# Kernel tuning notes

Measured on AMD Instinct MI355X. Metric: run time of the kernel, lower is better.

Reference implementation:

```python
import jax, jax.numpy as jnp
import numpy as np

FREQ_RES = 100.0 / 256.0
NUM_FILTERS = 6
_CFG = [(0.5, 4.0), (4.0, 8.0), (8.0, 12.0), (12.0, 16.0), (16.0, 24.0), (24.0, 30.0)]
BANDS = [(int(a / FREQ_RES), int(b / FREQ_RES)) for a, b in _CFG]  # (start_bin, end_bin)


def _interp_idx(n_src, n_dst):
    # torch F.interpolate bilinear, align_corners=False, along last dim (T dim is identity since same size)
    j = np.arange(n_dst)
    src = np.maximum((j + 0.5) * n_src / n_dst - 0.5, 0.0)
    x0 = np.floor(src).astype(np.int32)
    x1 = np.minimum(x0 + 1, n_src - 1)
    w = (src - x0).astype(np.float32)
    return x0, x1, w


def _gelu(x):
    return jax.nn.gelu(x, approximate=False)


def _forward(spec, centers, widths, gains, align_w, align_b, fc1_w, fc1_b, fc2_w, fc2_b,
             band_gain, gate_w, gate_b, proj_w, proj_b, bn_gamma, bn_beta, bn_mean, bn_var):
    B, C, T, F = spec.shape
    N = NUM_FILTERS
    band_feats = []
    for i, (s, e) in enumerate(BANDS):
        nb = e - s + 1
        sl = spec[:, :, :, s:e + 1]                       # [B,C,T,nb]
        mu = jax.nn.softplus(centers[i]) + s              # [C,N]
        mu = jnp.clip(mu, s, s + nb - 1)
        std = jnp.clip(jax.nn.softplus(widths[i]) + 1e-3, 0.5, 2.0 * nb / N)
        freqs = jnp.arange(nb, dtype=spec.dtype)          # relative bins [nb]
        g = jnp.exp(-0.5 * ((freqs[None, None, :] - mu[:, :, None]) / std[:, :, None]) ** 2)  # [C,N,nb]
        w = gains[i][:, :, None] * g / (g.sum(-1, keepdims=True) + 1e-6)
        filt = jnp.einsum('bctf,cnf->bctn', sl, w)        # [B,C,T,N]
        aligned = jnp.einsum('bctn,dc->bdtn', filt, align_w[i]) + align_b[i][None, :, None, None]
        band_feats.append(aligned)
    band_stack = jnp.stack(band_feats, axis=1)            # [B,6,C,T,N]
    nb_bands = band_stack.shape[1]
    x = band_stack.reshape(B, nb_bands * C, T, N)
    h = _gelu(jnp.einsum('bktn,ok->botn', x, fc1_w) + fc1_b[None, :, None, None])
    attn = jnp.einsum('botn,ko->bktn', h, fc2_w) + fc2_b[None, :, None, None]
    attn = jax.nn.softmax(attn.reshape(B, nb_bands, C, T, N), axis=1)  # softmax over bands
    band_stack = band_stack * attn * band_gain[None, :, None, None, None]
    enhanced = jnp.zeros_like(spec)
    for i, (s, e) in enumerate(BANDS):
        nb = e - s + 1
        narrow = band_stack[:, i]                         # [B,C,T,N]
        x0, x1, wl = _interp_idx(NUM_FILTERS, nb)
        wl = jnp.asarray(wl, dtype=spec.dtype)
        bf = narrow[..., x0] * (1.0 - wl) + narrow[..., x1] * wl   # [B,C,T,nb]
        enhanced = enhanced.at[:, :, :, s:e + 1].add(bf)
    residual = enhanced - spec
    gate = jax.nn.sigmoid(jnp.einsum('bctf,dc->bdtf', residual, gate_w) + gate_b[None, :, None, None])
    enhanced2 = spec + gate * residual
    y = jnp.einsum('bctf,dc->bdtf', enhanced2, proj_w) + proj_b[None, :, None, None]
    y = (y - bn_mean[None, :, None, None]) / jnp.sqrt(bn_var[None, :, None, None] + 1e-5)
    y = y * bn_gamma[None, :, None, None] + bn_beta[None, :, None, None]
    return _gelu(y)


def setup_inputs() -> dict:
    key = jax.random.key(0)
    ks = jax.random.split(key, 8)
    B, C, T, F, N = 64, 3, 3000, 103, NUM_FILTERS
    spec = jax.random.normal(ks[0], (B, C, T, F), dtype=jnp.float32)
    centers = jnp.stack([jnp.broadcast_to(jnp.linspace(a, b, N, dtype=jnp.float32) / FREQ_RES, (C, N)) for a, b in _CFG])
    widths = jnp.stack([jnp.full((C, N), (b - a) / N / FREQ_RES, dtype=jnp.float32) for a, b in _CFG])
    gains = jnp.ones((6, C, N), jnp.float32)
    align_w = jax.random.normal(ks[1], (6, C, C), dtype=jnp.float32) / np.sqrt(C)
    align_b = jax.random.normal(ks[2], (6, C), dtype=jnp.float32) * 0.02
    inter = 2 * C
    fc1_w = jax.random.normal(ks[3], (inter, 6 * C), dtype=jnp.float32) / np.sqrt(6 * C)
    fc1_b = jnp.zeros((inter,), jnp.float32)
    fc2_w = jax.random.normal(ks[4], (6 * C, inter), dtype=jnp.float32) / np.sqrt(inter)
    fc2_b = jnp.zeros((6 * C,), jnp.float32)
    band_gain = jnp.ones((6,), jnp.float32)
    gate_w = jax.random.normal(ks[5], (C, C), dtype=jnp.float32) / np.sqrt(C)
    gate_b = jnp.zeros((C,), jnp.float32)
    proj_w = jax.random.normal(ks[6], (C, C), dtype=jnp.float32) / np.sqrt(C)
    proj_b = jnp.zeros((C,), jnp.float32)
    bn_gamma = jnp.ones((C,), jnp.float32)
    bn_beta = jnp.zeros((C,), jnp.float32)
    bn_mean = jnp.zeros((C,), jnp.float32)
    bn_var = jnp.ones((C,), jnp.float32)
    return {"spec": spec, "centers": centers, "widths": widths, "gains": gains,
            "align_w": align_w, "align_b": align_b, "fc1_w": fc1_w, "fc1_b": fc1_b,
            "fc2_w": fc2_w, "fc2_b": fc2_b, "band_gain": band_gain,
            "gate_w": gate_w, "gate_b": gate_b, "proj_w": proj_w, "proj_b": proj_b,
            "bn_gamma": bn_gamma, "bn_beta": bn_beta, "bn_mean": bn_mean, "bn_var": bn_var}


def reference(spec, centers, widths, gains, align_w, align_b, fc1_w, fc1_b, fc2_w, fc2_b,
              band_gain, gate_w, gate_b, proj_w, proj_b, bn_gamma, bn_beta, bn_mean, bn_var):
    return _forward(spec, centers, widths, gains, align_w, align_b, fc1_w, fc1_b, fc2_w, fc2_b,
                    band_gain, gate_w, gate_b, proj_w, proj_b, bn_gamma, bn_beta, bn_mean, bn_var)
```

## Files before the change

### kernel.cpp

```cpp
#include <hip/hip_runtime.h>
#include <math.h>

namespace {

constexpr int C_ = 3, T_ = 3000, F_ = 103, NB_ = 6;
constexpr int TT = 20;
constexpr int NT = 3;
constexpr int BS[NB_]  = {1, 10, 20, 30, 40, 61};
constexpr int BNB[NB_] = {10, 11, 11, 11, 22, 16};
constexpr int WB[NB_]  = {0, 5, 11, 17, 23, 34};
constexpr int WBC[NB_] = {5, 6, 6, 6, 11, 8};
constexpr int WROW = 42;
constexpr int WTOTU = 18 * WROW;
constexpr int SPF = 81;
constexpr int PLANE = T_ * F_;
constexpr int SECP = 2064;
constexpr int POOL2 = 6192;

__device__ __forceinline__ float softplus_(float x) {
  return fmaxf(x, 0.0f) + log1pf(expf(-fabsf(x)));
}
__device__ __forceinline__ float sigmoid_(float z) {
  return 1.0f / (1.0f + __expf(-z));
}
__device__ __forceinline__ float gelu_(float x) {
  return x * sigmoid_(1.595769122f * x * (1.0f + 0.044715f * x * x));
}
__device__ __forceinline__ unsigned bf16_rne_(float x) {
  unsigned b = __float_as_uint(x);
  b += 0x7FFFu + ((b >> 16) & 1u);
  return b >> 16;
}

__global__ __launch_bounds__(128)
void prep_kernel(const float* __restrict__ centers,
                 const float* __restrict__ widths,
                 const float* __restrict__ gains,
                 const float* __restrict__ proj_w,
                 const float* __restrict__ proj_b,
                 const float* __restrict__ bn_gamma,
                 const float* __restrict__ bn_beta,
                 const float* __restrict__ bn_mean,
                 const float* __restrict__ bn_var,
                 float* __restrict__ ws)
{
  unsigned* wsU = (unsigned*)ws;
  const int q = threadIdx.x;
  if (q < 108) {
    int i = q / 18;
    int p = q - i * 18;
    int s = BS[i], nb = BNB[i];
    float mu = softplus_(centers[q]) + (float)s;
    mu = fminf(fmaxf(mu, (float)s), (float)(s + nb - 1));
    float sd = softplus_(widths[q]) + 0.001f;
    sd = fminf(fmaxf(sd, 0.5f), 2.0f * (float)nb / 6.0f);
    float sum = 0.0f;
    for (int f = 0; f < nb; ++f) {
      float d = ((float)f - mu) / sd;
      sum += __expf(-0.5f * d * d);
    }
    float sc = gains[q] / (sum + 1e-6f);
    float wtmp[22];
    for (int f = 0; f < nb; ++f) {
      float d = ((float)f - mu) / sd;
      wtmp[f] = sc * __expf(-0.5f * d * d);
    }
    const int wc = (nb + 1) / 2;
    for (int e = 0; e < wc; ++e) {
      unsigned lo = bf16_rne_(wtmp[2 * e]);
      unsigned hi = (2 * e + 1 < nb) ? bf16_rne_(wtmp[2 * e + 1]) : 0u;
      wsU[p * WROW + WB[i] + e] = lo | (hi << 16);
    }
  } else if (q < 117) {
    int k = q - 108, d = k / 3;
    float sc = bn_gamma[d] / sqrtf(bn_var[d] + 1e-5f);
    ws[WTOTU + k] = proj_w[k] * sc;
  } else if (q < 120) {
    int d = q - 117;
    float sc = bn_gamma[d] / sqrtf(bn_var[d] + 1e-5f);
    ws[WTOTU + 9 + d] = (proj_b[d] - bn_mean[d]) * sc + bn_beta[d];
  }
}

__global__ __launch_bounds__(256)
void sleepband_kernel(const float* __restrict__ spec,
                      const float* __restrict__ ws,
                      const float* __restrict__ align_w,
                      const float* __restrict__ align_b,
                      const float* __restrict__ fc1_w,
                      const float* __restrict__ fc1_b,
                      const float* __restrict__ fc2_w,
                      const float* __restrict__ fc2_b,
                      const float* __restrict__ band_gain,
                      const float* __restrict__ gate_w,
                      const float* __restrict__ gate_b,
                      float* __restrict__ out)
{
  __shared__ __align__(16) float sPool[POOL2];
  __shared__ unsigned sWu[WTOTU];
  __shared__ float sBand[TT][109];
  __shared__ float sAw[54], sAb[18], sF1[108], sF1b[6], sF2[108], sF2b[18],
                   sBg[6], sGw[9], sGb[3], sPw[9], sPb[3];

  const int tid = threadIdx.x;
  const int b   = blockIdx.y;
  const float* specB = spec + (size_t)b * C_ * PLANE;
  float* outBase = out + (size_t)b * C_ * PLANE;
  const unsigned* wsU = (const unsigned*)ws;

  for (int k = tid; k < WTOTU; k += 256) sWu[k] = wsU[k];
  if (tid < 54)  sAw[tid]  = align_w[tid];
  if (tid < 18)  sAb[tid]  = align_b[tid];
  if (tid < 108) sF1[tid]  = fc1_w[tid];
  if (tid < 6)   sF1b[tid] = fc1_b[tid];
  if (tid < 108) sF2[tid]  = fc2_w[tid];
  if (tid < 18)  sF2b[tid] = fc2_b[tid];
  if (tid < 6)   sBg[tid]  = band_gain[tid];
  if (tid < 9)   sGw[tid]  = gate_w[tid];
  if (tid < 3)   sGb[tid]  = gate_b[tid];
  if (tid < 9)   sPw[tid]  = ws[WTOTU + tid];
  if (tid < 3)   sPb[tid]  = ws[WTOTU + 9 + tid];

  for (int tile = 0; tile < NT; ++tile) {
    const int t0 = (blockIdx.x * NT + tile) * TT;

    for (int li = tid; li < C_ * TT * SPF; li += 256) {
      int c   = li / (TT * SPF);
      int rem = li - c * (TT * SPF);
      int tt  = rem / SPF;
      int f   = rem - tt * SPF;
      sPool[li] = specB[(size_t)c * PLANE + (size_t)(t0 + tt) * F_ + f];
    }
    __syncthreads();

    if (tid < 180) {
      const int g  = tid / TT;
      const int tt = tid - g * TT;
      const int c  = g / 3;
      const int np = g - c * 3;
      const int n0 = 2 * np;
      const float* srow = &sPool[(c * TT + tt) * SPF];
      const unsigned* w0 = &sWu[(c * 6 + n0) * WROW];
      const unsigned* w1 = w0 + WROW;
      #pragma unroll
      for (int i = 0; i < NB_; ++i) {
        const float* sr = srow + BS[i];
        float a0 = 0.0f, a1 = 0.0f;
        #pragma unroll
        for (int e = 0; e < WBC[i]; ++e) {
          float s0 = sr[2 * e], s1 = sr[2 * e + 1];
          unsigned u0 = w0[WB[i] + e], u1 = w1[WB[i] + e];
          a0 += s0 * __uint_as_float(u0 << 16);
          a0 += s1 * __uint_as_float(u0 & 0xffff0000u);
          a1 += s0 * __uint_as_float(u1 << 16);
          a1 += s1 * __uint_as_float(u1 & 0xffff0000u);
        }
        sBand[tt][(i * 3 + c) * 6 + n0]     = a0;
        sBand[tt][(i * 3 + c) * 6 + n0 + 1] = a1;
      }
    }
    __syncthreads();

    if (tid < 6 * TT) {
      int n  = tid / TT;
      int tt = tid - n * TT;
      float al[18];
      #pragma unroll
      for (int i = 0; i < 6; ++i) {
        float f0 = sBand[tt][(i * 3 + 0) * 6 + n];
        float f1 = sBand[tt][(i * 3 + 1) * 6 + n];
        float f2 = sBand[tt][(i * 3 + 2) * 6 + n];
        #pragma unroll
        for (int d = 0; d < 3; ++d)
          al[i * 3 + d] = sAw[i * 9 + d * 3 + 0] * f0 + sAw[i * 9 + d * 3 + 1] * f1 +
                          sAw[i * 9 + d * 3 + 2] * f2 + sAb[i * 3 + d];
      }
      float h[6];
      #pragma unroll
      for (int o = 0; o < 6; ++o) {
        float acc = sF1b[o];
        #pragma unroll
        for (int k = 0; k < 18; ++k) acc += sF1[o * 18 + k] * al[k];
        h[o] = gelu_(acc);
      }
      float at[18];
      #pragma unroll
      for (int k = 0; k < 18; ++k) {
        float acc = sF2b[k];
        #pragma unroll
        for (int o = 0; o < 6; ++o) acc += sF2[k * 6 + o] * h[o];
        at[k] = acc;
      }
      #pragma unroll
      for (int c = 0; c < 3; ++c) {
        float m = at[c];
        #pragma unroll
        for (int i = 1; i < 6; ++i) m = fmaxf(m, at[i * 3 + c]);
        float e[6], ssum = 0.0f;
        #pragma unroll
        for (int i = 0; i < 6; ++i) { e[i] = __expf(at[i * 3 + c] - m); ssum += e[i]; }
        float inv = 1.0f / ssum;
        #pragma unroll
        for (int i = 0; i < 6; ++i)
          sBand[tt][(i * 3 + c) * 6 + n] = al[i * 3 + c] * (e[i] * inv) * sBg[i];
      }
    }
    __syncthreads();

    if (tid < C_ * TT) {
      const int c  = tid / TT;
      const int tt = tid - c * TT;
      float bnd[36];
      #pragma unroll
      for (int i = 0; i < 6; ++i)
        #pragma unroll
        for (int n = 0; n < 6; ++n)
          bnd[i * 6 + n] = sBand[tt][(i * 3 + c) * 6 + n];
      float* row = &sPool[c * SECP + tt * F_];
      row[0] = 0.0f;
      float carry = 0.0f;
      #pragma unroll
      for (int i = 0; i < NB_; ++i) {
        #pragma unroll
        for (int j = 0; j < BNB[i]; ++j) {
          float src = ((float)j + 0.5f) * 6.0f / (float)BNB[i] - 0.5f;
          src = src > 0.0f ? src : 0.0f;
          int   x0 = (int)src;
          int   x1 = (x0 < 5) ? x0 + 1 : 5;
          float wl = src - (float)x0;
          float v  = bnd[i * 6 + x0] * (1.0f - wl) + bnd[i * 6 + x1] * wl;
          if (j == 0) v += carry;
          if (i < NB_ - 1 && j == BNB[i] - 1) carry = v;
          else row[BS[i] + j] = v;
        }
      }
      #pragma unroll
      for (int f = 77; f < F_; ++f) row[f] = 0.0f;
    }
    __syncthreads();

    float gw[9], pw[9], gb3[3], pb3[3];
    #pragma unroll
    for (int k = 0; k < 9; ++k) { gw[k] = sGw[k]; pw[k] = sPw[k]; }
    #pragma unroll
    for (int k = 0; k < 3; ++k) { gb3[k] = sGb[k]; pb3[k] = sPb[k]; }

    const float* sp0 = specB + (size_t)t0 * F_;
    float* outB = outBase + (size_t)t0 * F_;
    for (int e4 = tid; e4 < (TT * F_) / 4; e4 += 256) {
      const int e = e4 * 4;
      const float4 sA = *(const float4*)(sp0 + e);
      const float4 sB = *(const float4*)(sp0 + PLANE + e);
      const float4 sC = *(const float4*)(sp0 + 2 * PLANE + e);
      const float4 eA = *(const float4*)&sPool[0 * SECP + e];
      const float4 eB = *(const float4*)&sPool[1 * SECP + e];
      const float4 eC = *(const float4*)&sPool[2 * SECP + e];
      float4 oA, oB, oC;
      const float* sAp = (const float*)&sA; const float* sBp = (const float*)&sB;
      const float* sCp = (const float*)&sC;
      const float* eAp = (const float*)&eA; const float* eBp = (const float*)&eB;
      const float* eCp = (const float*)&eC;
      float* oAp = (float*)&oA; float* oBp = (float*)&oB; float* oCp = (float*)&oC;
      #pragma unroll
      for (int j = 0; j < 4; ++j) {
        float sv0 = sAp[j], sv1 = sBp[j], sv2 = sCp[j];
        float r0 = eAp[j] - sv0, r1 = eBp[j] - sv1, r2 = eCp[j] - sv2;
        float e20 = sv0 + sigmoid_(gw[0] * r0 + gw[1] * r1 + gw[2] * r2 + gb3[0]) * r0;
        float e21 = sv1 + sigmoid_(gw[3] * r0 + gw[4] * r1 + gw[5] * r2 + gb3[1]) * r1;
        float e22 = sv2 + sigmoid_(gw[6] * r0 + gw[7] * r1 + gw[8] * r2 + gb3[2]) * r2;
        float y0 = pw[0] * e20 + pw[1] * e21 + pw[2] * e22 + pb3[0];
        float y1 = pw[3] * e20 + pw[4] * e21 + pw[5] * e22 + pb3[1];
        float y2 = pw[6] * e20 + pw[7] * e21 + pw[8] * e22 + pb3[2];
        oAp[j] = gelu_(y0); oBp[j] = gelu_(y1); oCp[j] = gelu_(y2);
      }
      *(float4*)(outB + e) = oA;
      *(float4*)(outB + PLANE + e) = oB;
      *(float4*)(outB + 2 * PLANE + e) = oC;
    }
    __syncthreads();
  }
}

}

extern "C" void kernel_launch(void* const* d_in, const int* in_sizes, int n_in,
                              void* d_out, int out_size, void* d_ws, size_t ws_size,
                              hipStream_t stream) {
  (void)n_in; (void)out_size; (void)ws_size;
  const int B = in_sizes[0] / (C_ * T_ * F_);
  float* ws = (float*)d_ws;
  prep_kernel<<<1, 128, 0, stream>>>(
      (const float*)d_in[1],  (const float*)d_in[2],  (const float*)d_in[3],
      (const float*)d_in[13], (const float*)d_in[14], (const float*)d_in[15],
      (const float*)d_in[16], (const float*)d_in[17], (const float*)d_in[18], ws);
  dim3 grid(T_ / (TT * NT), B);
  sleepband_kernel<<<grid, 256, 0, stream>>>(
      (const float*)d_in[0],  ws,
      (const float*)d_in[4],  (const float*)d_in[5],
      (const float*)d_in[6],  (const float*)d_in[7],  (const float*)d_in[8],
      (const float*)d_in[9],  (const float*)d_in[10], (const float*)d_in[11],
      (const float*)d_in[12], (float*)d_out);
}
```

Baseline: 239.8 us.

## Prefetch next spec tile into registers and interpolate enhanced rows on the fly

Loads of the next time tile's spectrum slice now go into registers during the output pass, then into shared memory at the end of each tile. This overlaps global-load latency with compute and drops one barrier per tile. The separate pass that wrote interpolated enhanced rows to shared memory is replaced by per-frequency tap tables (column indices and weights), built once per block and evaluated inline in the output loop. This removes a serialized 60-thread stage and its barrier, at the cost of more shared-memory gathers per output element and extra register pressure from the staging array.

```diff
diff --git a/kernel.cpp b/kernel.cpp
--- a/kernel.cpp
+++ b/kernel.cpp
@@ -13,9 +13,9 @@
 constexpr int WROW = 42;
 constexpr int WTOTU = 18 * WROW;
 constexpr int SPF = 81;
+constexpr int SPECN = C_ * TT * SPF;
 constexpr int PLANE = T_ * F_;
-constexpr int SECP = 2064;
-constexpr int POOL2 = 6192;
+constexpr int NSTG = (SPECN + 255) / 256;
 
 __device__ __forceinline__ float softplus_(float x) {
   return fmaxf(x, 0.0f) + log1pf(expf(-fabsf(x)));
@@ -96,9 +96,11 @@
                       const float* __restrict__ gate_b,
                       float* __restrict__ out)
 {
-  __shared__ __align__(16) float sPool[POOL2];
+  __shared__ float sPool[SPECN];
   __shared__ unsigned sWu[WTOTU];
   __shared__ float sBand[TT][109];
+  __shared__ unsigned sTapC[F_];
+  __shared__ float sTapW[F_ * 5];
   __shared__ float sAw[54], sAb[18], sF1[108], sF1b[6], sF2[108], sF2b[18],
                    sBg[6], sGw[9], sGb[3], sPw[9], sPb[3];
 
@@ -107,7 +109,15 @@
   const float* specB = spec + (size_t)b * C_ * PLANE;
   float* outBase = out + (size_t)b * C_ * PLANE;
   const unsigned* wsU = (const unsigned*)ws;
-
+  const int tbase = blockIdx.x * NT * TT;
+
+  for (int li = tid; li < SPECN; li += 256) {
+    int c   = li / (TT * SPF);
+    int rem = li - c * (TT * SPF);
+    int tt  = rem / SPF;
+    int f   = rem - tt * SPF;
+    sPool[li] = specB[(size_t)c * PLANE + (size_t)(tbase + tt) * F_ + f];
+  }
   for (int k = tid; k < WTOTU; k += 256) sWu[k] = wsU[k];
   if (tid < 54)  sAw[tid]  = align_w[tid];
   if (tid < 18)  sAb[tid]  = align_b[tid];
@@ -120,18 +130,35 @@
   if (tid < 3)   sGb[tid]  = gate_b[tid];
   if (tid < 9)   sPw[tid]  = ws[WTOTU + tid];
   if (tid < 3)   sPb[tid]  = ws[WTOTU + 9 + tid];
+  if (tid < F_) {
+    const int f = tid;
+    unsigned cols = 0;
+    float w4[4] = {0.f, 0.f, 0.f, 0.f};
+    int slot = 0;
+    #pragma unroll
+    for (int i = 0; i < NB_; ++i) {
+      if (f >= BS[i] && f < BS[i] + BNB[i]) {
+        int j = f - BS[i];
+        float src = ((float)j + 0.5f) * 6.0f / (float)BNB[i] - 0.5f;
+        src = src > 0.0f ? src : 0.0f;
+        int x0 = (int)src;
+        int x1 = (x0 < 5) ? x0 + 1 : 5;
+        float wl = src - (float)x0;
+        cols |= ((unsigned)(i * 18 + x0) << (16 * slot))
+              | ((unsigned)(i * 18 + x1) << (16 * slot + 8));
+        w4[2 * slot] = 1.0f - wl;
+        w4[2 * slot + 1] = wl;
+        ++slot;
+      }
+    }
+    sTapC[f] = cols;
+    #pragma unroll
+    for (int q = 0; q < 4; ++q) sTapW[f * 5 + q] = w4[q];
+  }
+  __syncthreads();
 
   for (int tile = 0; tile < NT; ++tile) {
-    const int t0 = (blockIdx.x * NT + tile) * TT;
-
-    for (int li = tid; li < C_ * TT * SPF; li += 256) {
-      int c   = li / (TT * SPF);
-      int rem = li - c * (TT * SPF);
-      int tt  = rem / SPF;
-      int f   = rem - tt * SPF;
-      sPool[li] = specB[(size_t)c * PLANE + (size_t)(t0 + tt) * F_ + f];
-    }
-    __syncthreads();
+    const int t0 = tbase + tile * TT;
 
     if (tid < 180) {
       const int g  = tid / TT;
@@ -207,37 +234,22 @@
     }
     __syncthreads();
 
-    if (tid < C_ * TT) {
-      const int c  = tid / TT;
-      const int tt = tid - c * TT;
-      float bnd[36];
-      #pragma unroll
-      for (int i = 0; i < 6; ++i)
-        #pragma unroll
-        for (int n = 0; n < 6; ++n)
-          bnd[i * 6 + n] = sBand[tt][(i * 3 + c) * 6 + n];
-      float* row = &sPool[c * SECP + tt * F_];
-      row[0] = 0.0f;
-      float carry = 0.0f;
-      #pragma unroll
-      for (int i = 0; i < NB_; ++i) {
-        #pragma unroll
-        for (int j = 0; j < BNB[i]; ++j) {
-          float src = ((float)j + 0.5f) * 6.0f / (float)BNB[i] - 0.5f;
-          src = src > 0.0f ? src : 0.0f;
-          int   x0 = (int)src;
-          int   x1 = (x0 < 5) ? x0 + 1 : 5;
-          float wl = src - (float)x0;
-          float v  = bnd[i * 6 + x0] * (1.0f - wl) + bnd[i * 6 + x1] * wl;
-          if (j == 0) v += carry;
-          if (i < NB_ - 1 && j == BNB[i] - 1) carry = v;
-          else row[BS[i] + j] = v;
+    float rst[NSTG];
+    const bool more = (tile + 1 < NT);
+    if (more) {
+      const int t0n = t0 + TT;
+      #pragma unroll
+      for (int j = 0; j < NSTG; ++j) {
+        int li = tid + j * 256;
+        if (li < SPECN) {
+          int c   = li / (TT * SPF);
+          int rem = li - c * (TT * SPF);
+          int tt  = rem / SPF;
+          int f   = rem - tt * SPF;
+          rst[j] = specB[(size_t)c * PLANE + (size_t)(t0n + tt) * F_ + f];
         }
       }
-      #pragma unroll
-      for (int f = 77; f < F_; ++f) row[f] = 0.0f;
-    }
-    __syncthreads();
+    }
 
     float gw[9], pw[9], gb3[3], pb3[3];
     #pragma unroll
@@ -252,19 +264,26 @@
       const float4 sA = *(const float4*)(sp0 + e);
       const float4 sB = *(const float4*)(sp0 + PLANE + e);
       const float4 sC = *(const float4*)(sp0 + 2 * PLANE + e);
-      const float4 eA = *(const float4*)&sPool[0 * SECP + e];
-      const float4 eB = *(const float4*)&sPool[1 * SECP + e];
-      const float4 eC = *(const float4*)&sPool[2 * SECP + e];
       float4 oA, oB, oC;
       const float* sAp = (const float*)&sA; const float* sBp = (const float*)&sB;
       const float* sCp = (const float*)&sC;
-      const float* eAp = (const float*)&eA; const float* eBp = (const float*)&eB;
-      const float* eCp = (const float*)&eC;
       float* oAp = (float*)&oA; float* oBp = (float*)&oB; float* oCp = (float*)&oC;
       #pragma unroll
       for (int j = 0; j < 4; ++j) {
+        const int idx = e + j;
+        const int tt  = idx / F_;
+        const int f   = idx - tt * F_;
+        const unsigned cp = sTapC[f];
+        const float wa0 = sTapW[f * 5 + 0], wb0 = sTapW[f * 5 + 1];
+        const float wa1 = sTapW[f * 5 + 2], wb1 = sTapW[f * 5 + 3];
+        const float* br = &sBand[tt][0];
+        const int ca0 = cp & 0xffu, cb0 = (cp >> 8) & 0xffu;
+        const int ca1 = (cp >> 16) & 0xffu, cb1 = cp >> 24;
+        float e0 = wa0 * br[ca0]      + wb0 * br[cb0]      + wa1 * br[ca1]      + wb1 * br[cb1];
+        float e1 = wa0 * br[ca0 + 6]  + wb0 * br[cb0 + 6]  + wa1 * br[ca1 + 6]  + wb1 * br[cb1 + 6];
+        float e2 = wa0 * br[ca0 + 12] + wb0 * br[cb0 + 12] + wa1 * br[ca1 + 12] + wb1 * br[cb1 + 12];
         float sv0 = sAp[j], sv1 = sBp[j], sv2 = sCp[j];
-        float r0 = eAp[j] - sv0, r1 = eBp[j] - sv1, r2 = eCp[j] - sv2;
+        float r0 = e0 - sv0, r1 = e1 - sv1, r2 = e2 - sv2;
         float e20 = sv0 + sigmoid_(gw[0] * r0 + gw[1] * r1 + gw[2] * r2 + gb3[0]) * r0;
         float e21 = sv1 + sigmoid_(gw[3] * r0 + gw[4] * r1 + gw[5] * r2 + gb3[1]) * r1;
         float e22 = sv2 + sigmoid_(gw[6] * r0 + gw[7] * r1 + gw[8] * r2 + gb3[2]) * r2;
@@ -277,7 +296,15 @@
       *(float4*)(outB + PLANE + e) = oB;
       *(float4*)(outB + 2 * PLANE + e) = oC;
     }
-    __syncthreads();
+
+    if (more) {
+      #pragma unroll
+      for (int j = 0; j < NSTG; ++j) {
+        int li = tid + j * 256;
+        if (li < SPECN) sPool[li] = rst[j];
+      }
+      __syncthreads();
+    }
   }
 }
 
```

Result: slower. 284.2 us (+18.5%).

## Pack spectrum slice and enhanced rows as bf16 pairs in shared memory

Applied to the files above, without the earlier changes.

The staged spectrum slice and the enhanced-spectrum rows are now kept in LDS as packed bf16 pairs instead of fp32. The filter weights are realigned to even bin offsets so the dot products can read one packed word per two bins, and a minimum occupancy of 6 waves is requested through launch bounds. This roughly halves LDS use and staging traffic so more blocks fit per CU. The cost is extra rounding of activations to bf16, which loses precision, plus per-element index division and unpacking in the final epilogue.

```diff
diff --git a/kernel.cpp b/kernel.cpp
--- a/kernel.cpp
+++ b/kernel.cpp
@@ -8,14 +8,17 @@
 constexpr int NT = 3;
 constexpr int BS[NB_]  = {1, 10, 20, 30, 40, 61};
 constexpr int BNB[NB_] = {10, 11, 11, 11, 22, 16};
-constexpr int WB[NB_]  = {0, 5, 11, 17, 23, 34};
-constexpr int WBC[NB_] = {5, 6, 6, 6, 11, 8};
-constexpr int WROW = 42;
+constexpr int WSTART[NB_] = {0, 5, 10, 15, 20, 30};
+constexpr int WCNT[NB_]   = {6, 6, 6, 6, 11, 9};
+constexpr int WOFF[NB_]   = {0, 6, 12, 18, 24, 35};
+constexpr int WROW = 44;
 constexpr int WTOTU = 18 * WROW;
-constexpr int SPF = 81;
+constexpr int SPW = 39;
+constexpr int SPECW = C_ * TT * SPW;
+constexpr int ERS = 52;
+constexpr int EPL = TT * ERS;
+constexpr int POOLU = 3 * EPL;
 constexpr int PLANE = T_ * F_;
-constexpr int SECP = 2064;
-constexpr int POOL2 = 6192;
 
 __device__ __forceinline__ float softplus_(float x) {
   return fmaxf(x, 0.0f) + log1pf(expf(-fabsf(x)));
@@ -31,6 +34,8 @@
   b += 0x7FFFu + ((b >> 16) & 1u);
   return b >> 16;
 }
+__device__ __forceinline__ float bl_(unsigned u) { return __uint_as_float(u << 16); }
+__device__ __forceinline__ float bh_(unsigned u) { return __uint_as_float(u & 0xffff0000u); }
 
 __global__ __launch_bounds__(128)
 void prep_kernel(const float* __restrict__ centers,
@@ -65,11 +70,12 @@
       float d = ((float)f - mu) / sd;
       wtmp[f] = sc * __expf(-0.5f * d * d);
     }
-    const int wc = (nb + 1) / 2;
-    for (int e = 0; e < wc; ++e) {
-      unsigned lo = bf16_rne_(wtmp[2 * e]);
-      unsigned hi = (2 * e + 1 < nb) ? bf16_rne_(wtmp[2 * e + 1]) : 0u;
-      wsU[p * WROW + WB[i] + e] = lo | (hi << 16);
+    for (int e = 0; e < WCNT[i]; ++e) {
+      int flo = 2 * (WSTART[i] + e) - s;
+      int fhi = flo + 1;
+      unsigned lo = (flo >= 0 && flo < nb) ? bf16_rne_(wtmp[flo]) : 0u;
+      unsigned hi = (fhi >= 0 && fhi < nb) ? bf16_rne_(wtmp[fhi]) : 0u;
+      wsU[p * WROW + WOFF[i] + e] = lo | (hi << 16);
     }
   } else if (q < 117) {
     int k = q - 108, d = k / 3;
@@ -82,7 +88,7 @@
   }
 }
 
-__global__ __launch_bounds__(256)
+__global__ __launch_bounds__(256, 6)
 void sleepband_kernel(const float* __restrict__ spec,
                       const float* __restrict__ ws,
                       const float* __restrict__ align_w,
@@ -96,7 +102,7 @@
                       const float* __restrict__ gate_b,
                       float* __restrict__ out)
 {
-  __shared__ __align__(16) float sPool[POOL2];
+  __shared__ unsigned sPoolU[POOLU];
   __shared__ unsigned sWu[WTOTU];
   __shared__ float sBand[TT][109];
   __shared__ float sAw[54], sAb[18], sF1[108], sF1b[6], sF2[108], sF2b[18],
@@ -124,12 +130,15 @@
   for (int tile = 0; tile < NT; ++tile) {
     const int t0 = (blockIdx.x * NT + tile) * TT;
 
-    for (int li = tid; li < C_ * TT * SPF; li += 256) {
-      int c   = li / (TT * SPF);
-      int rem = li - c * (TT * SPF);
-      int tt  = rem / SPF;
-      int f   = rem - tt * SPF;
-      sPool[li] = specB[(size_t)c * PLANE + (size_t)(t0 + tt) * F_ + f];
+    for (int li = tid; li < SPECW; li += 256) {
+      int c   = li / (TT * SPW);
+      int rem = li - c * (TT * SPW);
+      int tt  = rem / SPW;
+      int w   = rem - tt * SPW;
+      const float* gr = specB + (size_t)c * PLANE + (size_t)(t0 + tt) * F_;
+      unsigned lo = bf16_rne_(gr[2 * w]);
+      unsigned hi = bf16_rne_(gr[2 * w + 1]);
+      sPoolU[li] = lo | (hi << 16);
     }
     __syncthreads();
 
@@ -139,21 +148,19 @@
       const int c  = g / 3;
       const int np = g - c * 3;
       const int n0 = 2 * np;
-      const float* srow = &sPool[(c * TT + tt) * SPF];
+      const unsigned* srow = &sPoolU[(c * TT + tt) * SPW];
       const unsigned* w0 = &sWu[(c * 6 + n0) * WROW];
       const unsigned* w1 = w0 + WROW;
       #pragma unroll
       for (int i = 0; i < NB_; ++i) {
-        const float* sr = srow + BS[i];
         float a0 = 0.0f, a1 = 0.0f;
         #pragma unroll
-        for (int e = 0; e < WBC[i]; ++e) {
-          float s0 = sr[2 * e], s1 = sr[2 * e + 1];
-          unsigned u0 = w0[WB[i] + e], u1 = w1[WB[i] + e];
-          a0 += s0 * __uint_as_float(u0 << 16);
-          a0 += s1 * __uint_as_float(u0 & 0xffff0000u);
-          a1 += s0 * __uint_as_float(u1 << 16);
-          a1 += s1 * __uint_as_float(u1 & 0xffff0000u);
+        for (int e = 0; e < WCNT[i]; ++e) {
+          unsigned su = srow[WSTART[i] + e];
+          float s0 = bl_(su), s1 = bh_(su);
+          unsigned u0 = w0[WOFF[i] + e], u1 = w1[WOFF[i] + e];
+          a0 += s0 * bl_(u0); a0 += s1 * bh_(u0);
+          a1 += s0 * bl_(u1); a1 += s1 * bh_(u1);
         }
         sBand[tt][(i * 3 + c) * 6 + n0]     = a0;
         sBand[tt][(i * 3 + c) * 6 + n0 + 1] = a1;
@@ -216,13 +223,14 @@
         #pragma unroll
         for (int n = 0; n < 6; ++n)
           bnd[i * 6 + n] = sBand[tt][(i * 3 + c) * 6 + n];
-      float* row = &sPool[c * SECP + tt * F_];
-      row[0] = 0.0f;
+      unsigned* rowU = &sPoolU[c * EPL + tt * ERS];
+      float pend = 0.0f;
       float carry = 0.0f;
       #pragma unroll
       for (int i = 0; i < NB_; ++i) {
         #pragma unroll
         for (int j = 0; j < BNB[i]; ++j) {
+          const int f = BS[i] + j;
           float src = ((float)j + 0.5f) * 6.0f / (float)BNB[i] - 0.5f;
           src = src > 0.0f ? src : 0.0f;
           int   x0 = (int)src;
@@ -230,12 +238,17 @@
           float wl = src - (float)x0;
           float v  = bnd[i * 6 + x0] * (1.0f - wl) + bnd[i * 6 + x1] * wl;
           if (j == 0) v += carry;
-          if (i < NB_ - 1 && j == BNB[i] - 1) carry = v;
-          else row[BS[i] + j] = v;
+          if (i < NB_ - 1 && j == BNB[i] - 1) {
+            carry = v;
+          } else {
+            if (f & 1) rowU[f >> 1] = bf16_rne_(pend) | (bf16_rne_(v) << 16);
+            else       pend = v;
+          }
         }
       }
-      #pragma unroll
-      for (int f = 77; f < F_; ++f) row[f] = 0.0f;
+      rowU[38] = bf16_rne_(pend);
+      #pragma unroll
+      for (int w = 39; w < ERS; ++w) rowU[w] = 0u;
     }
     __syncthreads();
 
@@ -252,19 +265,25 @@
       const float4 sA = *(const float4*)(sp0 + e);
       const float4 sB = *(const float4*)(sp0 + PLANE + e);
       const float4 sC = *(const float4*)(sp0 + 2 * PLANE + e);
-      const float4 eA = *(const float4*)&sPool[0 * SECP + e];
-      const float4 eB = *(const float4*)&sPool[1 * SECP + e];
-      const float4 eC = *(const float4*)&sPool[2 * SECP + e];
       float4 oA, oB, oC;
       const float* sAp = (const float*)&sA; const float* sBp = (const float*)&sB;
       const float* sCp = (const float*)&sC;
-      const float* eAp = (const float*)&eA; const float* eBp = (const float*)&eB;
-      const float* eCp = (const float*)&eC;
       float* oAp = (float*)&oA; float* oBp = (float*)&oB; float* oCp = (float*)&oC;
       #pragma unroll
       for (int j = 0; j < 4; ++j) {
+        const int idx = e + j;
+        const int tt  = idx / F_;
+        const int f   = idx - tt * F_;
+        const int wd  = tt * ERS + (f >> 1);
+        const unsigned ua = sPoolU[0 * EPL + wd];
+        const unsigned ub = sPoolU[1 * EPL + wd];
+        const unsigned uc = sPoolU[2 * EPL + wd];
+        const bool hi = (f & 1);
+        float e0 = hi ? bh_(ua) : bl_(ua);
+        float e1 = hi ? bh_(ub) : bl_(ub);
+        float e2 = hi ? bh_(uc) : bl_(uc);
         float sv0 = sAp[j], sv1 = sBp[j], sv2 = sCp[j];
-        float r0 = eAp[j] - sv0, r1 = eBp[j] - sv1, r2 = eCp[j] - sv2;
+        float r0 = e0 - sv0, r1 = e1 - sv1, r2 = e2 - sv2;
         float e20 = sv0 + sigmoid_(gw[0] * r0 + gw[1] * r1 + gw[2] * r2 + gb3[0]) * r0;
         float e21 = sv1 + sigmoid_(gw[3] * r0 + gw[4] * r1 + gw[5] * r2 + gb3[1]) * r1;
         float e22 = sv2 + sigmoid_(gw[6] * r0 + gw[7] * r1 + gw[8] * r2 + gb3[2]) * r2;
```

New measurement: 234.8 us, median of 2. 2.1% less time.
